# Performance work log

Hardware: AMD Instinct MI355X
Metric: run time of the kernel (lower is better)

## Reference

```python
import jax, jax.numpy as jnp
import numpy as np

NEG_SLOPE = 0.2  # PyG GATConv default negative_slope


def gat_conv(x, edge_index, W, a_src, a_dst, b):
    """PyG GATConv with add_self_loops=True, concat=False (mean over heads).
    x: [N, F_in]; W: [F_in, H*D]; a_src/a_dst: [H, D]; b: [D].
    Returns [N, D].
    """
    N = x.shape[0]
    H, D = a_src.shape
    xh = (x @ W).reshape(N, H, D)            # [N, H, D]
    loop = jnp.arange(N, dtype=edge_index.dtype)
    src = jnp.concatenate([edge_index[0], loop])  # [E+N]
    dst = jnp.concatenate([edge_index[1], loop])  # [E+N]
    # per-node attention logits
    asrc = jnp.einsum('nhd,hd->nh', xh, a_src)    # [N, H]
    adst = jnp.einsum('nhd,hd->nh', xh, a_dst)    # [N, H]
    e = asrc[src] + adst[dst]                      # [E+N, H]
    e = jnp.where(e > 0, e, NEG_SLOPE * e)         # LeakyReLU
    # softmax over incoming edges of each destination node
    emax = jax.ops.segment_max(e, dst, num_segments=N)   # [N, H]
    ex = jnp.exp(e - emax[dst])
    denom = jax.ops.segment_sum(ex, dst, num_segments=N) # [N, H]
    alpha = ex / denom[dst]                               # [E+N, H]
    # scatter-aggregate messages
    out = jax.ops.segment_sum(alpha[:, :, None] * xh[src], dst, num_segments=N)  # [N, H, D]
    return out.mean(axis=1) + b                           # concat=False -> mean heads


def setup_inputs() -> dict:
    key = jax.random.key(0)
    ks = jax.random.split(key, 10)
    N, F, D, C, H, E = 100000, 128, 32, 16, 8, 1600000
    s1 = 1.0 / np.sqrt(F)
    s2 = 1.0 / np.sqrt(D)
    return {
        'x': jax.random.normal(ks[0], (N, F), dtype=jnp.float32),
        'edge_index': jax.random.randint(ks[1], (2, E), 0, N, dtype=jnp.int32),
        'W1': jax.random.normal(ks[2], (F, H * D), dtype=jnp.float32) * s1,
        'a_src1': jax.random.normal(ks[3], (H, D), dtype=jnp.float32) * s2,
        'a_dst1': jax.random.normal(ks[4], (H, D), dtype=jnp.float32) * s2,
        'b1': jnp.zeros((D,), dtype=jnp.float32),
        'W2': jax.random.normal(ks[5], (D, H * C), dtype=jnp.float32) * s2,
        'a_src2': jax.random.normal(ks[6], (H, C), dtype=jnp.float32) * (1.0 / np.sqrt(C)),
        'a_dst2': jax.random.normal(ks[7], (H, C), dtype=jnp.float32) * (1.0 / np.sqrt(C)),
        'b2': jnp.zeros((C,), dtype=jnp.float32),
    }


def reference(x, edge_index, W1, a_src1, a_dst1, b1, W2, a_src2, a_dst2, b2):
    h = gat_conv(x, edge_index, W1, a_src1, a_dst1, b1)
    h = jax.nn.elu(h)                       # F.elu; Dropout(p=0.0) is identity
    logits = gat_conv(h, edge_index, W2, a_src2, a_dst2, b2)
    return (jax.nn.log_softmax(logits, axis=1), logits)
```

## Files before the change

kernel.cpp:

```cpp
#include <hip/hip_runtime.h>
#include <hip/hip_bf16.h>
#include <hip/hip_fp16.h>
#include <math.h>

#define LEAK 0.2f
#define BSTRIDE 64

typedef _Float16 f16;
typedef _Float16 f16x2 __attribute__((ext_vector_type(2)));
typedef _Float16 f16x4 __attribute__((ext_vector_type(4)));
typedef _Float16 f16x8 __attribute__((ext_vector_type(8)));
typedef float f32x2 __attribute__((ext_vector_type(2)));
typedef float f32x4 __attribute__((ext_vector_type(4)));

__global__ void transpose_w_k(const float* __restrict__ W, f16* __restrict__ Wt,
                              int K, int NC) {
  int idx = blockIdx.x * 256 + threadIdx.x;
  if (idx >= K * NC) return;
  int n = idx / K, k = idx - n * K;
  Wt[idx] = (f16)W[(size_t)k * NC + n];
}

template <int K, int BN, int DH, bool FILL>
__global__ __launch_bounds__(256) void gemm_att_mfma_k(
    const float* __restrict__ A, const f16* __restrict__ Bt,
    unsigned char* __restrict__ Cout, const float* __restrict__ a_src,
    const float* __restrict__ a_dst, float* __restrict__ asrc,
    float* __restrict__ adst, int M, int NC,
    const int* __restrict__ ei, int E, int Nn,
    unsigned* __restrict__ cnt, unsigned* __restrict__ bucket) {
  constexpr int CH = K / 8;
  constexpr int CT = BN / 16;
  __shared__ __align__(16) unsigned char smem[(64 + BN) * K * 2];
  f16* As = (f16*)smem;
  f16* Bs = (f16*)(smem + 64 * K * 2);
  unsigned char* stage = smem;
  const int tid = threadIdx.x;
  const int row0 = blockIdx.y * 64;
  const int col0 = blockIdx.x * BN;

#pragma unroll
  for (int it = 0; it < (64 * CH) / 256; ++it) {
    int idx = it * 256 + tid;
    int r = idx / CH, c = idx - r * CH;
    int grow = row0 + r;
    float4 v0 = make_float4(0.f, 0.f, 0.f, 0.f), v1 = v0;
    if (grow < M) {
      const float* gp = A + (size_t)grow * K + c * 8;
      v0 = *(const float4*)gp;
      v1 = *(const float4*)(gp + 4);
    }
    f16x8 h = {(f16)v0.x, (f16)v0.y, (f16)v0.z, (f16)v0.w,
               (f16)v1.x, (f16)v1.y, (f16)v1.z, (f16)v1.w};
    *(f16x8*)&As[r * K + (((c + r) & (CH - 1)) << 3)] = h;
  }
#pragma unroll
  for (int it = 0; it < (BN * CH) / 256; ++it) {
    int idx = it * 256 + tid;
    int n = idx / CH, c = idx - n * CH;
    f16x8 h = *(const f16x8*)(Bt + (size_t)(col0 + n) * K + c * 8);
    *(f16x8*)&Bs[n * K + (((c + n) & (CH - 1)) << 3)] = h;
  }
  __syncthreads();

  const int wv = tid >> 6;
  const int lane = tid & 63;
  const int l16 = lane & 15;
  const int l4 = lane >> 4;

  f32x4 acc[CT];
#pragma unroll
  for (int ct = 0; ct < CT; ++ct) acc[ct] = (f32x4){0.f, 0.f, 0.f, 0.f};

  const int ar = wv * 16 + l16;
#pragma unroll
  for (int kt = 0; kt < K / 32; ++kt) {
    int aj = kt * 4 + l4;
    f16x8 av = *(const f16x8*)&As[ar * K + (((aj + ar) & (CH - 1)) << 3)];
#pragma unroll
    for (int ct = 0; ct < CT; ++ct) {
      int br = ct * 16 + l16;
      f16x8 bv = *(const f16x8*)&Bs[br * K + (((aj + br) & (CH - 1)) << 3)];
      acc[ct] = __builtin_amdgcn_mfma_f32_16x16x32_f16(av, bv, acc[ct], 0, 0, 0);
    }
  }

  constexpr int HPB = BN / DH;
  constexpr int CTH = DH / 16;
  float ps[HPB][4], pd[HPB][4];
#pragma unroll
  for (int hl = 0; hl < HPB; ++hl)
#pragma unroll
    for (int r = 0; r < 4; ++r) { ps[hl][r] = 0.f; pd[hl][r] = 0.f; }

#pragma unroll
  for (int ct = 0; ct < CT; ++ct) {
    int col = col0 + ct * 16 + l16;
    float vs = a_src[col];
    float vd = a_dst[col];
    int hl = ct / CTH;
#pragma unroll
    for (int r = 0; r < 4; ++r) {
      ps[hl][r] += acc[ct][r] * vs;
      pd[hl][r] += acc[ct][r] * vd;
    }
  }

#pragma unroll
  for (int hl = 0; hl < HPB; ++hl) {
#pragma unroll
    for (int r = 0; r < 4; ++r) {
      float s = ps[hl][r], d = pd[hl][r];
#pragma unroll
      for (int m = 1; m < 16; m <<= 1) {
        s += __shfl_xor(s, m, 64);
        d += __shfl_xor(d, m, 64);
      }
      if (l16 == 0) {
        int grow = row0 + wv * 16 + l4 * 4 + r;
        int h = (col0 / DH) + hl;
        if (grow < M) {
          asrc[(size_t)grow * 8 + h] = s;
          adst[(size_t)grow * 8 + h] = d;
        }
      }
    }
  }

  __syncthreads();
  {
    const int j = lane & 3;
    const unsigned selAB = ((4u + j) << (8 * j)) | ((unsigned)j << (8 * (j ^ 1)));
    const unsigned selCD = ((4u + j) << (8 * (j ^ 2))) | ((unsigned)j << (8 * (j ^ 3)));
    const unsigned selMix =
        0x03020100u + (0x04040404u & ((j & 2) ? 0xFFFF0000u : 0x0000FFFFu));
    const int row = wv * 16 + l4 * 4 + j;
    const int colq = (l16 >> 2) * 4;
    const int swz = (row & 7) << 4;
#pragma unroll
    for (int ct = 0; ct < CT; ++ct) {
      unsigned wpk = (unsigned)__builtin_amdgcn_cvt_pk_fp8_f32(
          acc[ct][0], acc[ct][1], 0, false);
      wpk = (unsigned)__builtin_amdgcn_cvt_pk_fp8_f32(
          acc[ct][2], acc[ct][3], (int)wpk, true);
      unsigned Bx = (unsigned)__shfl_xor((int)wpk, 1, 64);
      unsigned Cx = (unsigned)__shfl_xor((int)wpk, 2, 64);
      unsigned Dx = (unsigned)__shfl_xor((int)wpk, 3, 64);
      unsigned P1 = __builtin_amdgcn_perm(wpk, Bx, selAB);
      unsigned P2 = __builtin_amdgcn_perm(Cx, Dx, selCD);
      unsigned ow = __builtin_amdgcn_perm(P1, P2, selMix);
      int colb = ct * 16 + colq;
      *(unsigned*)&stage[row * BN + (colb ^ swz)] = ow;
    }
  }
  __syncthreads();
  {
    constexpr int CPR = BN / 16;
#pragma unroll
    for (int i = 0; i < (64 * CPR) / 256; ++i) {
      int cid = i * 256 + tid;
      int row = cid / CPR, ch = cid - row * CPR;
      int grow = row0 + row;
      if (grow < M) {
        uint4 v = *(const uint4*)&stage[row * BN + ((ch * 16) ^ ((row & 7) << 4))];
        *(uint4*)(Cout + (size_t)grow * NC + col0 + ch * 16) = v;
      }
    }
  }

  if (FILL) {
    const int nthreads = (int)(gridDim.x * gridDim.y) * 256;
    const int Mtot = E + Nn;
    for (int p = (int)(blockIdx.y * gridDim.x + blockIdx.x) * 256 + tid;
         p < Mtot; p += nthreads) {
      int s, d;
      if (p < E) {
        s = ei[p];
        d = ei[E + p];
      } else {
        s = d = p - E;
      }
      unsigned pos = atomicAdd(&cnt[d], 1u);
      if (pos < BSTRIDE)
        __builtin_nontemporal_store((unsigned)s, &bucket[((size_t)d << 6) + pos]);
    }
  }
}

__global__ __launch_bounds__(256) void aggregate1_k(const unsigned char* __restrict__ xh8,
                                                    const float* __restrict__ asrc,
                                                    const float* __restrict__ adst,
                                                    const unsigned* __restrict__ cnt,
                                                    const unsigned* __restrict__ bucket,
                                                    const float* __restrict__ b1,
                                                    float* __restrict__ hout, int N) {
  __shared__ float wlds[4][64][8];
  __shared__ unsigned slds[4][64];
  const int lane = threadIdx.x & 63;
  const int wv = threadIdx.x >> 6;
  const int n = blockIdx.x * 4 + wv;
  const int nn = n < N ? n : N - 1;
  int deg = (int)cnt[nn];
  deg = deg > BSTRIDE ? BSTRIDE : deg;
  unsigned sv = bucket[((size_t)nn << 6) + lane];
  if (lane >= deg) sv = 0;

  float w[8];
  if (lane < deg) {
    const float4* ap = (const float4*)(asrc + (size_t)sv * 8);
    const float4* bp = (const float4*)(adst + (size_t)nn * 8);
    float4 a0 = ap[0], a1 = ap[1];
    float4 b0 = bp[0], b1v = bp[1];
    float e[8] = {a0.x + b0.x, a0.y + b0.y, a0.z + b0.z, a0.w + b0.w,
                  a1.x + b1v.x, a1.y + b1v.y, a1.z + b1v.z, a1.w + b1v.w};
#pragma unroll
    for (int j = 0; j < 8; ++j) {
      float t = e[j];
      t = t > 0.f ? t : LEAK * t;
      w[j] = __expf(t);
    }
  } else {
#pragma unroll
    for (int j = 0; j < 8; ++j) w[j] = 0.f;
  }
  *(float4*)&wlds[wv][lane][0] = make_float4(w[0], w[1], w[2], w[3]);
  *(float4*)&wlds[wv][lane][4] = make_float4(w[4], w[5], w[6], w[7]);
  slds[wv][lane] = sv;
  __syncthreads();
  if (n >= N) return;

  const int sub = lane >> 5;
  const int sl = lane & 31;
  const int h = sl >> 2;
  const uint2* xw = (const uint2*)xh8;

  float a0 = 0.f, a1 = 0.f, a2 = 0.f, a3 = 0.f;
  float a4 = 0.f, a5 = 0.f, a6 = 0.f, a7 = 0.f;
  float dsum = 0.f;
#pragma unroll 4
  for (int i = 0; i < deg; i += 2) {
    float w8 = wlds[wv][i + sub][h];
    unsigned s = slds[wv][i + sub];
    uint2 b = xw[(size_t)s * 32 + sl];
    f32x2 p0 = __builtin_amdgcn_cvt_pk_f32_fp8(b.x, false);
    f32x2 p1 = __builtin_amdgcn_cvt_pk_f32_fp8(b.x, true);
    f32x2 p2 = __builtin_amdgcn_cvt_pk_f32_fp8(b.y, false);
    f32x2 p3 = __builtin_amdgcn_cvt_pk_f32_fp8(b.y, true);
    a0 += w8 * p0.x; a1 += w8 * p0.y; a2 += w8 * p1.x; a3 += w8 * p1.y;
    a4 += w8 * p2.x; a5 += w8 * p2.y; a6 += w8 * p3.x; a7 += w8 * p3.y;
    dsum += w8;
  }

  a0 += __shfl_xor(a0, 32, 64); a1 += __shfl_xor(a1, 32, 64);
  a2 += __shfl_xor(a2, 32, 64); a3 += __shfl_xor(a3, 32, 64);
  a4 += __shfl_xor(a4, 32, 64); a5 += __shfl_xor(a5, 32, 64);
  a6 += __shfl_xor(a6, 32, 64); a7 += __shfl_xor(a7, 32, 64);
  dsum += __shfl_xor(dsum, 32, 64);

  float rinv = 0.125f * __builtin_amdgcn_rcpf(dsum);
  a0 *= rinv; a1 *= rinv; a2 *= rinv; a3 *= rinv;
  a4 *= rinv; a5 *= rinv; a6 *= rinv; a7 *= rinv;

#pragma unroll
  for (int m = 16; m >= 4; m >>= 1) {
    a0 += __shfl_xor(a0, m, 64); a1 += __shfl_xor(a1, m, 64);
    a2 += __shfl_xor(a2, m, 64); a3 += __shfl_xor(a3, m, 64);
    a4 += __shfl_xor(a4, m, 64); a5 += __shfl_xor(a5, m, 64);
    a6 += __shfl_xor(a6, m, 64); a7 += __shfl_xor(a7, m, 64);
  }
  if (lane < 4) {
    int d = lane * 8;
    float4 bv0 = *(const float4*)(b1 + d);
    float4 bv1 = *(const float4*)(b1 + d + 4);
    float o0 = a0 + bv0.x, o1 = a1 + bv0.y, o2 = a2 + bv0.z, o3 = a3 + bv0.w;
    float o4 = a4 + bv1.x, o5 = a5 + bv1.y, o6 = a6 + bv1.z, o7 = a7 + bv1.w;
    o0 = o0 > 0.f ? o0 : expm1f(o0);
    o1 = o1 > 0.f ? o1 : expm1f(o1);
    o2 = o2 > 0.f ? o2 : expm1f(o2);
    o3 = o3 > 0.f ? o3 : expm1f(o3);
    o4 = o4 > 0.f ? o4 : expm1f(o4);
    o5 = o5 > 0.f ? o5 : expm1f(o5);
    o6 = o6 > 0.f ? o6 : expm1f(o6);
    o7 = o7 > 0.f ? o7 : expm1f(o7);
    *(float4*)(hout + (size_t)n * 32 + d) = make_float4(o0, o1, o2, o3);
    *(float4*)(hout + (size_t)n * 32 + d + 4) = make_float4(o4, o5, o6, o7);
  }
}

__global__ __launch_bounds__(256) void aggregate2_k(const unsigned char* __restrict__ xq,
                                                    const float* __restrict__ asrc,
                                                    const float* __restrict__ adst,
                                                    const unsigned* __restrict__ cnt,
                                                    const unsigned* __restrict__ bucket,
                                                    const float* __restrict__ b2,
                                                    float* __restrict__ out, int N) {
  __shared__ float wlds[4][64][8];
  __shared__ unsigned slds[4][64];
  const int lane = threadIdx.x & 63;
  const int wv = threadIdx.x >> 6;
  const int n = blockIdx.x * 4 + wv;
  const int nn = n < N ? n : N - 1;
  int deg = (int)cnt[nn];
  deg = deg > BSTRIDE ? BSTRIDE : deg;
  unsigned sv = bucket[((size_t)nn << 6) + lane];
  if (lane >= deg) sv = 0;

  float w[8];
  if (lane < deg) {
    const float4* ap = (const float4*)(asrc + (size_t)sv * 8);
    const float4* bp = (const float4*)(adst + (size_t)nn * 8);
    float4 a0 = ap[0], a1 = ap[1];
    float4 b0 = bp[0], b1v = bp[1];
    float e[8] = {a0.x + b0.x, a0.y + b0.y, a0.z + b0.z, a0.w + b0.w,
                  a1.x + b1v.x, a1.y + b1v.y, a1.z + b1v.z, a1.w + b1v.w};
#pragma unroll
    for (int j = 0; j < 8; ++j) {
      float t = e[j];
      t = t > 0.f ? t : LEAK * t;
      w[j] = __expf(t);
    }
  } else {
#pragma unroll
    for (int j = 0; j < 8; ++j) w[j] = 0.f;
  }
  *(float4*)&wlds[wv][lane][0] = make_float4(w[0], w[1], w[2], w[3]);
  *(float4*)&wlds[wv][lane][4] = make_float4(w[4], w[5], w[6], w[7]);
  slds[wv][lane] = sv;
  __syncthreads();
  if (n >= N) return;

  const int sub = lane >> 5;
  const int sl = lane & 31;
  const int h = sl >> 2;
  const unsigned* xw = (const unsigned*)xq;

  float a0 = 0.f, a1 = 0.f, a2 = 0.f, a3 = 0.f;
  float dsum = 0.f;
#pragma unroll 4
  for (int i = 0; i < deg; i += 2) {
    float w8 = wlds[wv][i + sub][h];
    unsigned s = slds[wv][i + sub];
    unsigned b = xw[(size_t)s * 32 + sl];
    f32x2 p0 = __builtin_amdgcn_cvt_pk_f32_fp8(b, false);
    f32x2 p1 = __builtin_amdgcn_cvt_pk_f32_fp8(b, true);
    a0 += w8 * p0.x; a1 += w8 * p0.y; a2 += w8 * p1.x; a3 += w8 * p1.y;
    dsum += w8;
  }

  a0 += __shfl_xor(a0, 32, 64); a1 += __shfl_xor(a1, 32, 64);
  a2 += __shfl_xor(a2, 32, 64); a3 += __shfl_xor(a3, 32, 64);
  dsum += __shfl_xor(dsum, 32, 64);

  float rinv = 0.125f * __builtin_amdgcn_rcpf(dsum);
  a0 *= rinv; a1 *= rinv; a2 *= rinv; a3 *= rinv;

#pragma unroll
  for (int m = 16; m >= 4; m >>= 1) {
    a0 += __shfl_xor(a0, m, 64); a1 += __shfl_xor(a1, m, 64);
    a2 += __shfl_xor(a2, m, 64); a3 += __shfl_xor(a3, m, 64);
  }
  int c = (lane & 3) * 4;
  float4 bv = *(const float4*)(b2 + c);
  float l0 = a0 + bv.x, l1 = a1 + bv.y, l2 = a2 + bv.z, l3 = a3 + bv.w;

  float mx = fmaxf(fmaxf(l0, l1), fmaxf(l2, l3));
  mx = fmaxf(mx, __shfl_xor(mx, 1, 64));
  mx = fmaxf(mx, __shfl_xor(mx, 2, 64));
  float es = __expf(l0 - mx) + __expf(l1 - mx) + __expf(l2 - mx) + __expf(l3 - mx);
  es += __shfl_xor(es, 1, 64);
  es += __shfl_xor(es, 2, 64);
  float lse = logf(es) + mx;

  if (lane < 4) {
    *(float4*)(out + (size_t)n * 16 + c) = make_float4(l0 - lse, l1 - lse, l2 - lse, l3 - lse);
    *(float4*)(out + (size_t)N * 16 + (size_t)n * 16 + c) = make_float4(l0, l1, l2, l3);
  }
}

extern "C" void kernel_launch(void* const* d_in, const int* in_sizes, int n_in,
                              void* d_out, int out_size, void* d_ws, size_t ws_size,
                              hipStream_t stream) {
  const float* x      = (const float*)d_in[0];
  const int*   ei     = (const int*)d_in[1];
  const float* W1     = (const float*)d_in[2];
  const float* a_src1 = (const float*)d_in[3];
  const float* a_dst1 = (const float*)d_in[4];
  const float* b1     = (const float*)d_in[5];
  const float* W2     = (const float*)d_in[6];
  const float* a_src2 = (const float*)d_in[7];
  const float* a_dst2 = (const float*)d_in[8];
  const float* b2     = (const float*)d_in[9];

  const int N = in_sizes[0] / 128;
  const int E = in_sizes[1] / 2;

  char* w = (char*)d_ws;
  size_t used = 0;
  auto alloc = [&](size_t bytes) -> void* {
    size_t aligned = (bytes + 255) & ~(size_t)255;
    void* p = w + used;
    used += aligned;
    return p;
  };
  unsigned char* xh1q = (unsigned char*)alloc((size_t)N * 256);
  unsigned char* xh2q = xh1q;
  float*    hbuf   = (float*)alloc((size_t)N * 32 * 4);
  float*    asrc   = (float*)alloc((size_t)N * 8 * 4);
  float*    adst   = (float*)alloc((size_t)N * 8 * 4);
  unsigned* cnt    = (unsigned*)alloc((size_t)N * 4);
  unsigned* bucket = (unsigned*)alloc((size_t)N * BSTRIDE * 4);
  f16*      w1t    = (f16*)alloc((size_t)128 * 256 * 2);
  f16*      w2t    = (f16*)alloc((size_t)32 * 128 * 2);
  (void)ws_size;

  float* out = (float*)d_out;
  const int gy = (N + 63) / 64;

  transpose_w_k<<<(128 * 256 + 255) / 256, 256, 0, stream>>>(W1, w1t, 128, 256);
  transpose_w_k<<<(32 * 128 + 255) / 256, 256, 0, stream>>>(W2, w2t, 32, 128);
  hipMemsetAsync(cnt, 0, (size_t)N * 4, stream);

  gemm_att_mfma_k<128, 128, 32, true><<<dim3(2, gy), 256, 0, stream>>>(
      x, w1t, xh1q, a_src1, a_dst1, asrc, adst, N, 256, ei, E, N, cnt, bucket);

  aggregate1_k<<<(N + 3) / 4, 256, 0, stream>>>(xh1q, asrc, adst, cnt, bucket, b1, hbuf, N);

  gemm_att_mfma_k<32, 128, 16, false><<<dim3(1, gy), 256, 0, stream>>>(
      hbuf, w2t, xh2q, a_src2, a_dst2, asrc, adst, N, 128, nullptr, 0, 0, nullptr, nullptr);
  aggregate2_k<<<(N + 3) / 4, 256, 0, stream>>>(xh2q, asrc, adst, cnt, bucket, b2, out, N);
}
```

Measured before the change: 401.3 us.

## Split CSR bucket fill into its own kernel and load GEMM A-fragments directly into registers

The edge-bucket fill (atomic count plus scatter of source ids) moves out of the layer-1 GEMM epilogue into a separate one-thread-per-edge kernel. The GEMM now loads and converts its A tile straight from global memory into per-lane MFMA fragments, skipping the LDS A staging. This shrinks LDS so more blocks can be resident. The cost is an extra kernel launch, plus the GEMM can no longer hide the atomic fill work behind its own execution.

```diff
diff --git a/kernel.cpp b/kernel.cpp
--- a/kernel.cpp
+++ b/kernel.cpp
@@ -7,8 +7,6 @@
 #define BSTRIDE 64
 
 typedef _Float16 f16;
-typedef _Float16 f16x2 __attribute__((ext_vector_type(2)));
-typedef _Float16 f16x4 __attribute__((ext_vector_type(4)));
 typedef _Float16 f16x8 __attribute__((ext_vector_type(8)));
 typedef float f32x2 __attribute__((ext_vector_type(2)));
 typedef float f32x4 __attribute__((ext_vector_type(4)));
@@ -21,39 +19,41 @@
   Wt[idx] = (f16)W[(size_t)k * NC + n];
 }
 
-template <int K, int BN, int DH, bool FILL>
+__global__ __launch_bounds__(256) void fill_k(const int* __restrict__ ei, int E,
+                                              int Nn, unsigned* __restrict__ cnt,
+                                              unsigned* __restrict__ bucket) {
+  int p = blockIdx.x * 256 + threadIdx.x;
+  const int Mtot = E + Nn;
+  if (p >= Mtot) return;
+  int s, d;
+  if (p < E) {
+    s = ei[p];
+    d = ei[E + p];
+  } else {
+    s = d = p - E;
+  }
+  unsigned pos = atomicAdd(&cnt[d], 1u);
+  if (pos < BSTRIDE)
+    __builtin_nontemporal_store((unsigned)s, &bucket[((size_t)d << 6) + pos]);
+}
+
+template <int K, int BN, int DH>
 __global__ __launch_bounds__(256) void gemm_att_mfma_k(
     const float* __restrict__ A, const f16* __restrict__ Bt,
     unsigned char* __restrict__ Cout, const float* __restrict__ a_src,
     const float* __restrict__ a_dst, float* __restrict__ asrc,
-    float* __restrict__ adst, int M, int NC,
-    const int* __restrict__ ei, int E, int Nn,
-    unsigned* __restrict__ cnt, unsigned* __restrict__ bucket) {
+    float* __restrict__ adst, int M, int NC) {
   constexpr int CH = K / 8;
   constexpr int CT = BN / 16;
-  __shared__ __align__(16) unsigned char smem[(64 + BN) * K * 2];
-  f16* As = (f16*)smem;
-  f16* Bs = (f16*)(smem + 64 * K * 2);
+  constexpr int KT = K / 32;
+  constexpr int LDSB = (BN * K * 2) > (64 * BN) ? (BN * K * 2) : (64 * BN);
+  __shared__ __align__(16) unsigned char smem[LDSB];
+  f16* Bs = (f16*)smem;
   unsigned char* stage = smem;
   const int tid = threadIdx.x;
   const int row0 = blockIdx.y * 64;
   const int col0 = blockIdx.x * BN;
 
-#pragma unroll
-  for (int it = 0; it < (64 * CH) / 256; ++it) {
-    int idx = it * 256 + tid;
-    int r = idx / CH, c = idx - r * CH;
-    int grow = row0 + r;
-    float4 v0 = make_float4(0.f, 0.f, 0.f, 0.f), v1 = v0;
-    if (grow < M) {
-      const float* gp = A + (size_t)grow * K + c * 8;
-      v0 = *(const float4*)gp;
-      v1 = *(const float4*)(gp + 4);
-    }
-    f16x8 h = {(f16)v0.x, (f16)v0.y, (f16)v0.z, (f16)v0.w,
-               (f16)v1.x, (f16)v1.y, (f16)v1.z, (f16)v1.w};
-    *(f16x8*)&As[r * K + (((c + r) & (CH - 1)) << 3)] = h;
-  }
 #pragma unroll
   for (int it = 0; it < (BN * CH) / 256; ++it) {
     int idx = it * 256 + tid;
@@ -61,27 +61,40 @@
     f16x8 h = *(const f16x8*)(Bt + (size_t)(col0 + n) * K + c * 8);
     *(f16x8*)&Bs[n * K + (((c + n) & (CH - 1)) << 3)] = h;
   }
-  __syncthreads();
 
   const int wv = tid >> 6;
   const int lane = tid & 63;
   const int l16 = lane & 15;
   const int l4 = lane >> 4;
 
+  const int arow = row0 + wv * 16 + l16;
+  const bool aok = arow < M;
+  f16x8 afrag[KT];
+#pragma unroll
+  for (int kt = 0; kt < KT; ++kt) {
+    float4 v0 = make_float4(0.f, 0.f, 0.f, 0.f), v1 = v0;
+    if (aok) {
+      const float* gp = A + (size_t)arow * K + (kt * 4 + l4) * 8;
+      v0 = *(const float4*)gp;
+      v1 = *(const float4*)(gp + 4);
+    }
+    afrag[kt] = {(f16)v0.x, (f16)v0.y, (f16)v0.z, (f16)v0.w,
+                 (f16)v1.x, (f16)v1.y, (f16)v1.z, (f16)v1.w};
+  }
+  __syncthreads();
+
   f32x4 acc[CT];
 #pragma unroll
   for (int ct = 0; ct < CT; ++ct) acc[ct] = (f32x4){0.f, 0.f, 0.f, 0.f};
 
-  const int ar = wv * 16 + l16;
-#pragma unroll
-  for (int kt = 0; kt < K / 32; ++kt) {
+#pragma unroll
+  for (int kt = 0; kt < KT; ++kt) {
     int aj = kt * 4 + l4;
-    f16x8 av = *(const f16x8*)&As[ar * K + (((aj + ar) & (CH - 1)) << 3)];
 #pragma unroll
     for (int ct = 0; ct < CT; ++ct) {
       int br = ct * 16 + l16;
       f16x8 bv = *(const f16x8*)&Bs[br * K + (((aj + br) & (CH - 1)) << 3)];
-      acc[ct] = __builtin_amdgcn_mfma_f32_16x16x32_f16(av, bv, acc[ct], 0, 0, 0);
+      acc[ct] = __builtin_amdgcn_mfma_f32_16x16x32_f16(afrag[kt], bv, acc[ct], 0, 0, 0);
     }
   }
 
@@ -165,24 +178,6 @@
         uint4 v = *(const uint4*)&stage[row * BN + ((ch * 16) ^ ((row & 7) << 4))];
         *(uint4*)(Cout + (size_t)grow * NC + col0 + ch * 16) = v;
       }
-    }
-  }
-
-  if (FILL) {
-    const int nthreads = (int)(gridDim.x * gridDim.y) * 256;
-    const int Mtot = E + Nn;
-    for (int p = (int)(blockIdx.y * gridDim.x + blockIdx.x) * 256 + tid;
-         p < Mtot; p += nthreads) {
-      int s, d;
-      if (p < E) {
-        s = ei[p];
-        d = ei[E + p];
-      } else {
-        s = d = p - E;
-      }
-      unsigned pos = atomicAdd(&cnt[d], 1u);
-      if (pos < BSTRIDE)
-        __builtin_nontemporal_store((unsigned)s, &bucket[((size_t)d << 6) + pos]);
     }
   }
 }
@@ -416,16 +411,18 @@
   float* out = (float*)d_out;
   const int gy = (N + 63) / 64;
 
+  hipMemsetAsync(cnt, 0, (size_t)N * 4, stream);
   transpose_w_k<<<(128 * 256 + 255) / 256, 256, 0, stream>>>(W1, w1t, 128, 256);
   transpose_w_k<<<(32 * 128 + 255) / 256, 256, 0, stream>>>(W2, w2t, 32, 128);
-  hipMemsetAsync(cnt, 0, (size_t)N * 4, stream);
-
-  gemm_att_mfma_k<128, 128, 32, true><<<dim3(2, gy), 256, 0, stream>>>(
-      x, w1t, xh1q, a_src1, a_dst1, asrc, adst, N, 256, ei, E, N, cnt, bucket);
+
+  fill_k<<<(E + N + 255) / 256, 256, 0, stream>>>(ei, E, N, cnt, bucket);
+
+  gemm_att_mfma_k<128, 128, 32><<<dim3(2, gy), 256, 0, stream>>>(
+      x, w1t, xh1q, a_src1, a_dst1, asrc, adst, N, 256);
 
   aggregate1_k<<<(N + 3) / 4, 256, 0, stream>>>(xh1q, asrc, adst, cnt, bucket, b1, hbuf, N);
 
-  gemm_att_mfma_k<32, 128, 16, false><<<dim3(1, gy), 256, 0, stream>>>(
-      hbuf, w2t, xh2q, a_src2, a_dst2, asrc, adst, N, 128, nullptr, 0, 0, nullptr, nullptr);
+  gemm_att_mfma_k<32, 128, 16><<<dim3(1, gy), 256, 0, stream>>>(
+      hbuf, w2t, xh2q, a_src2, a_dst2, asrc, adst, N, 128);
   aggregate2_k<<<(N + 3) / 4, 256, 0, stream>>>(xh2q, asrc, adst, cnt, bucket, b2, out, N);
 }
```

Result: slower. 449.6 us (+12.0%).
